# Performance work log

Measured on AMD Instinct MI355X. Metric: run time of the kernel, lower is better.

## Reference

```python
import jax, jax.numpy as jnp
import numpy as np

N, E, FS = 50000, 400000, 256
H, D = 8, 64            # GAT heads, hidden_size (per-head out_feats)
NH, DK, DV = 8, 64, 64  # transformer MHA
B = 1024
NEG_SLOPE = 0.2
EPS = 1e-6


def _layer_norm(x, g, b, eps=EPS):
    mu = x.mean(-1, keepdims=True)
    var = x.var(-1, keepdims=True)
    return (x - mu) / jnp.sqrt(var + eps) * g + b


def setup_inputs() -> dict:
    key = jax.random.key(0)
    ks = jax.random.split(key, 20)
    s = 0.02
    return {
        "features": jax.random.normal(ks[0], (N, FS), jnp.float32),
        "src": jax.random.randint(ks[1], (E,), 0, N, jnp.int32),
        "dst": jax.random.randint(ks[2], (E,), 0, N, jnp.int32),
        "url": jax.random.randint(ks[3], (B,), 1, N + 1, jnp.int32),  # 1-based ids
        # GATConv params (DGL-style)
        "gat_fc_w": jax.random.normal(ks[4], (FS, H * D), jnp.float32) * s,
        "attn_l": jax.random.normal(ks[5], (H, D), jnp.float32) * s,
        "attn_r": jax.random.normal(ks[6], (H, D), jnp.float32) * s,
        "gat_res_w": jax.random.normal(ks[7], (FS, H * D), jnp.float32) * s,
        "gat_bias": jnp.zeros((H, D), jnp.float32),
        # post-GAT LayerNorm
        "ln_g": jnp.ones((D,), jnp.float32),
        "ln_b": jnp.zeros((D,), jnp.float32),
        # MultiHeadAttention params
        "wq": jax.random.normal(ks[8], (D, NH * DK), jnp.float32) * s,
        "wk": jax.random.normal(ks[9], (D, NH * DK), jnp.float32) * s,
        "wv": jax.random.normal(ks[10], (D, NH * DV), jnp.float32) * s,
        "fc_w": jax.random.normal(ks[11], (NH * DV, D), jnp.float32) * s,
        "fc_b": jnp.zeros((D,), jnp.float32),
        "mha_ln_g": jnp.ones((D,), jnp.float32),
        "mha_ln_b": jnp.zeros((D,), jnp.float32),
        # final classifier
        "out_w": jax.random.normal(ks[12], (D, 2), jnp.float32) * s,
        "out_b": jnp.zeros((2,), jnp.float32),
    }


def reference(features, src, dst, url, gat_fc_w, attn_l, attn_r, gat_res_w,
              gat_bias, ln_g, ln_b, wq, wk, wv, fc_w, fc_b, mha_ln_g,
              mha_ln_b, out_w, out_b):
    # ---- GATConv (residual=True, bias, negative_slope=0.2, no activation) ----
    feat = (features @ gat_fc_w).reshape(N, H, D)          # [N,H,D]
    el = jnp.einsum('nhd,hd->nh', feat, attn_l)            # [N,H]
    er = jnp.einsum('nhd,hd->nh', feat, attn_r)            # [N,H]
    e = jax.nn.leaky_relu(el[src] + er[dst], NEG_SLOPE)    # [E,H] edge scores
    # segment softmax over incoming edges of each dst node
    m = jax.ops.segment_max(e, dst, num_segments=N)        # [N,H]
    m = jnp.where(jnp.isfinite(m), m, 0.0)
    ex = jnp.exp(e - m[dst])                               # [E,H]
    denom = jax.ops.segment_sum(ex, dst, num_segments=N)   # [N,H]
    a = ex / jnp.maximum(denom[dst], 1e-20)                # [E,H]
    msg = feat[src] * a[:, :, None]                        # [E,H,D]
    rst = jax.ops.segment_sum(msg, dst, num_segments=N)    # [N,H,D]
    res = (features @ gat_res_w).reshape(N, H, D)
    gat_emb = rst + res + gat_bias                         # [N,H,D]

    # ---- select batch nodes (url is 1-based) ----
    ids = url - 1
    x = gat_emb[ids]                                       # [B,H,D]
    x = _layer_norm(x, ln_g, ln_b)

    # ---- dense multi-head self-attention over the H gat heads (seq dim) ----
    residual = x
    q = (x @ wq).reshape(B, H, NH, DK)
    k = (x @ wk).reshape(B, H, NH, DK)
    v = (x @ wv).reshape(B, H, NH, DV)
    attn = jnp.einsum('bqhd,bkhd->bhqk', q, k) / jnp.sqrt(jnp.float32(DK))
    attn = jax.nn.softmax(attn, axis=-1)
    o = jnp.einsum('bhqk,bkhd->bqhd', attn, v).reshape(B, H, NH * DV)
    o = o @ fc_w + fc_b                                    # [B,H,D]
    o = _layer_norm(o + residual, mha_ln_g, mha_ln_b)

    # ---- pool + classify ----
    pooled = o.sum(axis=1)                                 # [B,D]
    logits = pooled @ out_w + out_b                        # [B,2]
    return logits
```

## Files before the change

kernel.cpp:

```cpp
#include <hip/hip_runtime.h>
#include <math.h>

#define Nn 50000
#define Ee 400000
#define FSz 256
#define HD_ 512
#define Bb 1024

static __device__ __forceinline__ int clampi(int v, int lo, int hi){
    return v < lo ? lo : (v > hi ? hi : v);
}
static __device__ __forceinline__ unsigned short f2bf(float f){
    unsigned int u = __float_as_uint(f);
    unsigned int r = u + 0x7FFFu + ((u >> 16) & 1u);
    return (unsigned short)(r >> 16);
}
static __device__ __forceinline__ float bflo(unsigned int v){ return __uint_as_float(v << 16); }
static __device__ __forceinline__ float bfhi(unsigned int v){ return __uint_as_float(v & 0xFFFF0000u); }

__global__ __launch_bounds__(256) void k_init(int* uid, int* fill, int* cnt,
                                              const float* __restrict__ W,
                                              const float* __restrict__ al,
                                              const float* __restrict__ ar,
                                              float* __restrict__ wl, float* __restrict__ wr){
    int t = threadIdx.x;
    if(blockIdx.x == 196){
        __shared__ float sal[512], sar[512];
        sal[t] = al[t]; sal[t+256] = al[t+256];
        sar[t] = ar[t]; sar[t+256] = ar[t+256];
        __syncthreads();
        const float4* Wr = (const float4*)(W + t*512);
        float accl[8] = {0,0,0,0,0,0,0,0};
        float accr[8] = {0,0,0,0,0,0,0,0};
        for(int i = 0; i < 128; i++){
            float4 w = Wr[i];
            int o = 4*i;
            int h = o >> 6;
            const float* alp = &sal[o];
            const float* arp = &sar[o];
            accl[h] += w.x*alp[0] + w.y*alp[1] + w.z*alp[2] + w.w*alp[3];
            accr[h] += w.x*arp[0] + w.y*arp[1] + w.z*arp[2] + w.w*arp[3];
        }
        #pragma unroll
        for(int h = 0; h < 8; h++){ wl[h*256 + t] = accl[h]; wr[h*256 + t] = accr[h]; }
    } else {
        int i = blockIdx.x * 256 + t;
        if(i < Nn) uid[i] = -1;
        if(i < 1024) fill[i] = 0;
        if(i == 0) cnt[0] = 0;
    }
}

__global__ __launch_bounds__(256) void k_mark(const int* __restrict__ url, int* uid, int* unode, int* cnt){
    int b = blockIdx.x * 256 + threadIdx.x;
    if(b >= Bb) return;
    int n = clampi(url[b] - 1, 0, Nn - 1);
    int old = atomicCAS(&uid[n], -1, -2);
    if(old == -1){
        int id = atomicAdd(cnt, 1);
        unode[id] = n;
        uid[n] = id;
    }
}

__global__ __launch_bounds__(256) void k_scatter(const int* __restrict__ src, const int* __restrict__ dst,
                                                 const int* __restrict__ uid, int* __restrict__ fill,
                                                 int* __restrict__ slist){
    int e = blockIdx.x * 256 + threadIdx.x;
    if(e >= Ee) return;
    int d = dst[e];
    if((unsigned)d >= (unsigned)Nn) return;
    int u = uid[d];
    if(u < 0) return;
    int pos = atomicAdd(&fill[u], 1);
    if(pos >= 64) return;
    slist[u*64 + pos] = clampi(src[e], 0, Nn - 1);
}

__global__ __launch_bounds__(256) void k_gat(const float* __restrict__ features,
                                             const float* __restrict__ Wfc,
                                             const float* __restrict__ Wres,
                                             const float* __restrict__ bias,
                                             const float* __restrict__ wl,
                                             const float* __restrict__ wr,
                                             const int* __restrict__ cnt, const int* __restrict__ unode,
                                             const int* __restrict__ fill, const int* __restrict__ slist,
                                             float* __restrict__ gemb){
    int t = threadIdx.x;
    int lane = t & 63, wv = t >> 6;
    int cntv = cnt[0];
    int u0 = blockIdx.x * 2;
    if(u0 >= cntv) return;

    __shared__ float swl[2048], swr[2048];
    __shared__ float cxs[2][8][256];
    __shared__ float fres[2][256];
    __shared__ float sew[2][64][8];
    __shared__ float ser[2][8];
    __shared__ int   sslist[2][64];

    for(int i = t; i < 2048; i += 256){ swl[i] = wl[i]; swr[i] = wr[i]; }

    int dg[2];
    dg[0] = min(fill[u0], 64);
    dg[1] = (u0 + 1 < cntv) ? min(fill[u0 + 1], 64) : 0;
    #pragma unroll
    for(int j = 0; j < 2; j++){
        int u = u0 + j;
        if(t < dg[j]) sslist[j][t] = slist[u*64 + t];
        if(u < cntv) fres[j][t] = features[(size_t)unode[u] * FSz + t];
        else         fres[j][t] = 0.f;
    }
    __syncthreads();

    int total = dg[0] + dg[1];
    for(int tau = wv; tau < total + 2; tau += 4){
        int j, i, s, isEr;
        if(tau < dg[0]){ j = 0; i = tau; s = sslist[0][i]; isEr = 0; }
        else if(tau < total){ j = 1; i = tau - dg[0]; s = sslist[1][i]; isEr = 0; }
        else { j = tau - total; i = 0; s = (u0 + j < cntv) ? unode[u0 + j] : 0; isEr = 1; }
        float4 x = *(const float4*)(features + (size_t)s * FSz + 4*lane);
        const float* Wt = isEr ? swr : swl;
        float p[8];
        #pragma unroll
        for(int h = 0; h < 8; h++){
            float4 w = *(const float4*)&Wt[h*256 + 4*lane];
            p[h] = x.x*w.x + x.y*w.y + x.z*w.z + x.w*w.w;
        }
        #pragma unroll
        for(int h = 0; h < 8; h++){
            #pragma unroll
            for(int m = 32; m >= 1; m >>= 1) p[h] += __shfl_xor(p[h], m, 64);
        }
        if(lane == 0){
            if(isEr){
                #pragma unroll
                for(int h = 0; h < 8; h++) ser[j][h] = p[h];
            } else {
                #pragma unroll
                for(int h = 0; h < 8; h++) sew[j][i][h] = p[h];
            }
        }
    }
    __syncthreads();
    if(t < 16){
        int j = t >> 3, h = t & 7;
        int dgj = dg[j];
        if(dgj > 0){
            float ern = ser[j][h];
            float m = -1e30f;
            for(int i = 0; i < dgj; i++){
                float v = sew[j][i][h] + ern;
                v = v > 0.f ? v : 0.2f * v;
                m = fmaxf(m, v);
            }
            float sum = 0.f;
            for(int i = 0; i < dgj; i++){
                float v = sew[j][i][h] + ern;
                v = v > 0.f ? v : 0.2f * v;
                float w = expf(v - m);
                sum += w;
                sew[j][i][h] = w;
            }
            float inv = 1.0f / fmaxf(sum, 1e-20f);
            for(int i = 0; i < dgj; i++) sew[j][i][h] *= inv;
        }
    }
    __syncthreads();
    #pragma unroll
    for(int j = 0; j < 2; j++){
        float cx[8] = {0,0,0,0,0,0,0,0};
        for(int i = 0; i < dg[j]; i++){
            int s = sslist[j][i];
            float x = features[(size_t)s * FSz + t];
            const float* av = &sew[j][i][0];
            #pragma unroll
            for(int h = 0; h < 8; h++) cx[h] += av[h] * x;
        }
        #pragma unroll
        for(int h = 0; h < 8; h++) cxs[j][h][t] = cx[h];
    }
    __syncthreads();

    int h = t >> 5;
    int o0 = 2 * t;
    const float2* Wfc2  = (const float2*)Wfc;
    const float2* Wres2 = (const float2*)Wres;
    float a00 = 0.f, a01 = 0.f, a10 = 0.f, a11 = 0.f;
    for(int f = 0; f < 256; f += 4){
        float2 w0 = Wfc2[(f+0)*256 + t];
        float2 w1 = Wfc2[(f+1)*256 + t];
        float2 w2 = Wfc2[(f+2)*256 + t];
        float2 w3 = Wfc2[(f+3)*256 + t];
        float2 r0 = Wres2[(f+0)*256 + t];
        float2 r1 = Wres2[(f+1)*256 + t];
        float2 r2 = Wres2[(f+2)*256 + t];
        float2 r3 = Wres2[(f+3)*256 + t];
        float4 c0 = *(const float4*)&cxs[0][h][f];
        float4 x0 = *(const float4*)&fres[0][f];
        float4 c1 = *(const float4*)&cxs[1][h][f];
        float4 x1 = *(const float4*)&fres[1][f];
        a00 += c0.x*w0.x + c0.y*w1.x + c0.z*w2.x + c0.w*w3.x + x0.x*r0.x + x0.y*r1.x + x0.z*r2.x + x0.w*r3.x;
        a01 += c0.x*w0.y + c0.y*w1.y + c0.z*w2.y + c0.w*w3.y + x0.x*r0.y + x0.y*r1.y + x0.z*r2.y + x0.w*r3.y;
        a10 += c1.x*w0.x + c1.y*w1.x + c1.z*w2.x + c1.w*w3.x + x1.x*r0.x + x1.y*r1.x + x1.z*r2.x + x1.w*r3.x;
        a11 += c1.x*w0.y + c1.y*w1.y + c1.z*w2.y + c1.w*w3.y + x1.x*r0.y + x1.y*r1.y + x1.z*r2.y + x1.w*r3.y;
    }
    float b0 = bias[o0], b1 = bias[o0 + 1];
    {
        float2* gp = (float2*)(gemb + (size_t)u0 * HD_);
        gp[t] = make_float2(a00 + b0, a01 + b1);
    }
    if(u0 + 1 < cntv){
        float2* gp = (float2*)(gemb + (size_t)(u0 + 1) * HD_);
        gp[t] = make_float2(a10 + b0, a11 + b1);
    }
}

__global__ __launch_bounds__(256, 6) void k_mha(const int* __restrict__ url, const int* __restrict__ uid,
                                             const float* __restrict__ gemb,
                                             const float* __restrict__ lng, const float* __restrict__ lnb,
                                             const float* __restrict__ wq, const float* __restrict__ wk,
                                             const float* __restrict__ wvp, const float* __restrict__ fcw,
                                             const float* __restrict__ fcb, const float* __restrict__ mlg,
                                             const float* __restrict__ mlb, const float* __restrict__ outw,
                                             const float* __restrict__ outb, float* __restrict__ out){
    __shared__ float A[512];
    __shared__ float xnF[512];
    __shared__ unsigned short xnT[64*8];
    __shared__ unsigned short qkb[2*8*520];
    __shared__ float mu8[8], rs8[8], pooled[64];

    int b = blockIdx.x, t = threadIdx.x;
    int lane = t & 63, wv = t >> 6;
    int n = clampi(url[b] - 1, 0, Nn - 1);
    int u = uid[n];
    if(u < 0) u = 0;
    const float* gp = gemb + (size_t)u * HD_;
    A[t] = gp[t]; A[t + 256] = gp[t + 256];
    __syncthreads();
    if(t < 8){
        float s = 0.f, s2 = 0.f;
        for(int d = 0; d < 64; d++){ float v = A[t*64 + d]; s += v; s2 += v * v; }
        float mu = s * (1.0f/64.0f);
        float var = s2 * (1.0f/64.0f) - mu * mu;
        mu8[t] = mu; rs8[t] = rsqrtf(fmaxf(var, 0.0f) + 1e-6f);
    }
    __syncthreads();
    #pragma unroll
    for(int p = 0; p < 2; p++){
        int i = p*256 + t; int q = i >> 6, d = i & 63;
        float xv = (A[i] - mu8[q]) * rs8[q] * lng[d] + lnb[d];
        xnF[i] = xv;
        xnT[d*8 + q] = f2bf(xv);
    }
    __syncthreads();
    float aq0[8] = {0,0,0,0,0,0,0,0}, aq1[8] = {0,0,0,0,0,0,0,0};
    float ak0[8] = {0,0,0,0,0,0,0,0}, ak1[8] = {0,0,0,0,0,0,0,0};
    #pragma unroll 4
    for(int d = 0; d < 64; d++){
        float q0 = wq[d*512 + t], q1 = wq[d*512 + t + 256];
        float k0 = wk[d*512 + t], k1 = wk[d*512 + t + 256];
        uint4 xp = *(const uint4*)&xnT[d*8];
        float xv[8] = { bflo(xp.x), bfhi(xp.x), bflo(xp.y), bfhi(xp.y),
                        bflo(xp.z), bfhi(xp.z), bflo(xp.w), bfhi(xp.w) };
        #pragma unroll
        for(int r = 0; r < 8; r++){
            aq0[r] += xv[r]*q0; aq1[r] += xv[r]*q1;
            ak0[r] += xv[r]*k0; ak1[r] += xv[r]*k1;
        }
    }
    #pragma unroll
    for(int qq = 0; qq < 8; qq++){
        qkb[qq*520 + t]              = f2bf(aq0[qq]);
        qkb[qq*520 + t + 256]        = f2bf(aq1[qq]);
        qkb[4160 + qq*520 + t]       = f2bf(ak0[qq]);
        qkb[4160 + qq*520 + t + 256] = f2bf(ak1[qq]);
    }
    __syncthreads();
    #pragma unroll
    for(int p = 0; p < 2; p++){
        int idx = p*256 + t;
        int nh = idx >> 6, qq = (idx >> 3) & 7, kk = idx & 7;
        const unsigned short* qrow = &qkb[qq*520 + nh*64];
        const unsigned short* krow = &qkb[4160 + kk*520 + nh*64];
        float s = 0.f;
        #pragma unroll
        for(int d8 = 0; d8 < 64; d8 += 8){
            uint4 qv = *(const uint4*)&qrow[d8];
            uint4 kv = *(const uint4*)&krow[d8];
            s += bflo(qv.x)*bflo(kv.x) + bfhi(qv.x)*bfhi(kv.x)
               + bflo(qv.y)*bflo(kv.y) + bfhi(qv.y)*bfhi(kv.y)
               + bflo(qv.z)*bflo(kv.z) + bfhi(qv.z)*bfhi(kv.z)
               + bflo(qv.w)*bflo(kv.w) + bfhi(qv.w)*bfhi(kv.w);
        }
        A[idx] = s * 0.125f;
    }
    __syncthreads();
    if(t < 64){
        float mx = -1e30f;
        #pragma unroll
        for(int k = 0; k < 8; k++) mx = fmaxf(mx, A[t*8 + k]);
        float e[8]; float s = 0.f;
        #pragma unroll
        for(int k = 0; k < 8; k++){ e[k] = expf(A[t*8 + k] - mx); s += e[k]; }
        float inv = 1.0f / s;
        #pragma unroll
        for(int k = 0; k < 8; k++) A[t*8 + k] = e[k] * inv;
    }
    __syncthreads();
    float av0[8] = {0,0,0,0,0,0,0,0}, av1[8] = {0,0,0,0,0,0,0,0};
    #pragma unroll 4
    for(int d = 0; d < 64; d++){
        float v0 = wvp[d*512 + t], v1 = wvp[d*512 + t + 256];
        uint4 xp = *(const uint4*)&xnT[d*8];
        float xv[8] = { bflo(xp.x), bfhi(xp.x), bflo(xp.y), bfhi(xp.y),
                        bflo(xp.z), bfhi(xp.z), bflo(xp.w), bfhi(xp.w) };
        #pragma unroll
        for(int r = 0; r < 8; r++){ av0[r] += xv[r]*v0; av1[r] += xv[r]*v1; }
    }
    {
        int nh0 = wv;
        #pragma unroll
        for(int qq = 0; qq < 8; qq++){
            const float* s0 = &A[nh0*64 + qq*8];
            const float* s1 = &A[(nh0+4)*64 + qq*8];
            float4 a0 = *(const float4*)s0, b0 = *(const float4*)(s0 + 4);
            float4 a1 = *(const float4*)s1, b1 = *(const float4*)(s1 + 4);
            float o0 = a0.x*av0[0] + a0.y*av0[1] + a0.z*av0[2] + a0.w*av0[3]
                     + b0.x*av0[4] + b0.y*av0[5] + b0.z*av0[6] + b0.w*av0[7];
            float o1 = a1.x*av1[0] + a1.y*av1[1] + a1.z*av1[2] + a1.w*av1[3]
                     + b1.x*av1[4] + b1.y*av1[5] + b1.z*av1[6] + b1.w*av1[7];
            qkb[qq*520 + t]       = f2bf(o0);
            qkb[qq*520 + t + 256] = f2bf(o1);
        }
    }
    __syncthreads();
    {
        float* P = (float*)&qkb[4160];
        int g = lane & 31;
        int qh = lane >> 5;
        int k0 = wv * 128;
        float a[4][2] = {{0,0},{0,0},{0,0},{0,0}};
        const float2* fw2 = (const float2*)fcw;
        for(int k = k0; k < k0 + 128; k += 8){
            float2 f0 = fw2[(k+0)*32 + g];
            float2 f1 = fw2[(k+1)*32 + g];
            float2 f2 = fw2[(k+2)*32 + g];
            float2 f3 = fw2[(k+3)*32 + g];
            float2 f4 = fw2[(k+4)*32 + g];
            float2 f5 = fw2[(k+5)*32 + g];
            float2 f6 = fw2[(k+6)*32 + g];
            float2 f7 = fw2[(k+7)*32 + g];
            #pragma unroll
            for(int jq = 0; jq < 4; jq++){
                int qq = qh*4 + jq;
                uint4 op = *(const uint4*)&qkb[qq*520 + k];
                float x0 = bflo(op.x), x1 = bfhi(op.x), x2 = bflo(op.y), x3 = bfhi(op.y);
                float x4 = bflo(op.z), x5 = bfhi(op.z), x6 = bflo(op.w), x7 = bfhi(op.w);
                a[jq][0] += x0*f0.x + x1*f1.x + x2*f2.x + x3*f3.x + x4*f4.x + x5*f5.x + x6*f6.x + x7*f7.x;
                a[jq][1] += x0*f0.y + x1*f1.y + x2*f2.y + x3*f3.y + x4*f4.y + x5*f5.y + x6*f6.y + x7*f7.y;
            }
        }
        __syncthreads();
        #pragma unroll
        for(int jq = 0; jq < 4; jq++){
            int qq = qh*4 + jq;
            *(float2*)&P[wv*512 + qq*64 + 2*g] = make_float2(a[jq][0], a[jq][1]);
        }
        __syncthreads();
        #pragma unroll
        for(int p = 0; p < 2; p++){
            int o = p*256 + t;
            int dd = o & 63;
            A[o] = P[o] + P[512 + o] + P[1024 + o] + P[1536 + o] + fcb[dd] + xnF[o];
        }
    }
    __syncthreads();
    if(t < 8){
        float s = 0.f, s2 = 0.f;
        for(int d = 0; d < 64; d++){ float v = A[t*64 + d]; s += v; s2 += v * v; }
        float mu = s * (1.0f/64.0f);
        float var = s2 * (1.0f/64.0f) - mu * mu;
        mu8[t] = mu; rs8[t] = rsqrtf(fmaxf(var, 0.0f) + 1e-6f);
    }
    __syncthreads();
    if(t < 64){
        float g2 = mlg[t], bb = mlb[t];
        float s = 0.f;
        #pragma unroll
        for(int qq = 0; qq < 8; qq++)
            s += (A[qq*64 + t] - mu8[qq]) * rs8[qq] * g2 + bb;
        pooled[t] = s;
    }
    __syncthreads();
    if(t < 2){
        float s = outb[t];
        for(int d = 0; d < 64; d++) s += pooled[d] * outw[d*2 + t];
        out[b*2 + t] = s;
    }
}

extern "C" void kernel_launch(void* const* d_in, const int* in_sizes, int n_in,
                              void* d_out, int out_size, void* d_ws, size_t ws_size,
                              hipStream_t stream){
    (void)in_sizes; (void)n_in; (void)out_size; (void)ws_size;
    const float* features  = (const float*)d_in[0];
    const int*   src       = (const int*)d_in[1];
    const int*   dst       = (const int*)d_in[2];
    const int*   url       = (const int*)d_in[3];
    const float* gat_fc_w  = (const float*)d_in[4];
    const float* attn_l    = (const float*)d_in[5];
    const float* attn_r    = (const float*)d_in[6];
    const float* gat_res_w = (const float*)d_in[7];
    const float* gat_bias  = (const float*)d_in[8];
    const float* ln_g      = (const float*)d_in[9];
    const float* ln_b      = (const float*)d_in[10];
    const float* wq        = (const float*)d_in[11];
    const float* wk        = (const float*)d_in[12];
    const float* wv        = (const float*)d_in[13];
    const float* fc_w      = (const float*)d_in[14];
    const float* fc_b      = (const float*)d_in[15];
    const float* mha_ln_g  = (const float*)d_in[16];
    const float* mha_ln_b  = (const float*)d_in[17];
    const float* out_w     = (const float*)d_in[18];
    const float* out_b     = (const float*)d_in[19];

    char* base = (char*)d_ws;
    size_t cur = 0;
    auto alloc = [&](size_t nbytes) -> void* {
        void* p = base + cur;
        cur = (cur + nbytes + 255) & ~(size_t)255;
        return p;
    };
    float* wl    = (float*)alloc(2048 * sizeof(float));
    float* wr    = (float*)alloc(2048 * sizeof(float));
    int*   uid   = (int*)alloc((size_t)Nn * sizeof(int));
    int*   unode = (int*)alloc(1024 * sizeof(int));
    int*   cnt   = (int*)alloc(16);
    int*   fill  = (int*)alloc(1024 * sizeof(int));
    int*   slist = (int*)alloc((size_t)1024 * 64 * sizeof(int));
    float* gemb  = (float*)alloc((size_t)1024 * 512 * sizeof(float));

    hipLaunchKernelGGL(k_init,    dim3(197),  dim3(256), 0, stream, uid, fill, cnt,
                       gat_fc_w, attn_l, attn_r, wl, wr);
    hipLaunchKernelGGL(k_mark,    dim3(4),    dim3(256), 0, stream, url, uid, unode, cnt);
    hipLaunchKernelGGL(k_scatter, dim3(1563), dim3(256), 0, stream, src, dst, uid, fill, slist);
    hipLaunchKernelGGL(k_gat,     dim3(512),  dim3(256), 0, stream, features, gat_fc_w, gat_res_w, gat_bias,
                       wl, wr, cnt, unode, fill, slist, gemb);
    hipLaunchKernelGGL(k_mha,     dim3(1024), dim3(256), 0, stream, url, uid, gemb, ln_g, ln_b,
                       wq, wk, wv, fc_w, fc_b, mha_ln_g, mha_ln_b, out_w, out_b,
                       (float*)d_out);
}
```

Baseline: 242.8 us.

## Merge init into mark, keep attention weights in registers, fuse V projection

Workspace initialisation moves from the k_init kernel to two hipMemsetAsync calls, and the attention-weight precompute moves into the k_mark launch, so one kernel launch is removed. In k_gat, the wl/wr vectors are held in per-lane registers instead of being staged through shared memory. In k_mha, the V projection is folded into the Q/K projection loop so x is read once, and launch bounds drop from 6 to 4 waves so the extra accumulators fit in registers. The trade-off is higher register pressure and lower occupancy in k_mha and k_gat, plus memset calls whose cost is not the same as a kernel's.

```diff
diff --git a/kernel.cpp b/kernel.cpp
--- a/kernel.cpp
+++ b/kernel.cpp
@@ -18,13 +18,13 @@
 static __device__ __forceinline__ float bflo(unsigned int v){ return __uint_as_float(v << 16); }
 static __device__ __forceinline__ float bfhi(unsigned int v){ return __uint_as_float(v & 0xFFFF0000u); }
 
-__global__ __launch_bounds__(256) void k_init(int* uid, int* fill, int* cnt,
+__global__ __launch_bounds__(256) void k_mark(const int* __restrict__ url, int* uid, int* unode, int* cnt,
                                               const float* __restrict__ W,
                                               const float* __restrict__ al,
                                               const float* __restrict__ ar,
                                               float* __restrict__ wl, float* __restrict__ wr){
     int t = threadIdx.x;
-    if(blockIdx.x == 196){
+    if(blockIdx.x == 4){
         __shared__ float sal[512], sar[512];
         sal[t] = al[t]; sal[t+256] = al[t+256];
         sar[t] = ar[t]; sar[t+256] = ar[t+256];
@@ -44,22 +44,16 @@
         #pragma unroll
         for(int h = 0; h < 8; h++){ wl[h*256 + t] = accl[h]; wr[h*256 + t] = accr[h]; }
     } else {
-        int i = blockIdx.x * 256 + t;
-        if(i < Nn) uid[i] = -1;
-        if(i < 1024) fill[i] = 0;
-        if(i == 0) cnt[0] = 0;
-    }
-}
-
-__global__ __launch_bounds__(256) void k_mark(const int* __restrict__ url, int* uid, int* unode, int* cnt){
-    int b = blockIdx.x * 256 + threadIdx.x;
-    if(b >= Bb) return;
-    int n = clampi(url[b] - 1, 0, Nn - 1);
-    int old = atomicCAS(&uid[n], -1, -2);
-    if(old == -1){
-        int id = atomicAdd(cnt, 1);
-        unode[id] = n;
-        uid[n] = id;
+        int b = blockIdx.x * 256 + t;
+        if(b < Bb){
+            int n = clampi(url[b] - 1, 0, Nn - 1);
+            int old = atomicCAS(&uid[n], -1, -2);
+            if(old == -1){
+                int id = atomicAdd(cnt, 1);
+                unode[id] = n;
+                uid[n] = id;
+            }
+        }
     }
 }
 
@@ -92,14 +86,18 @@
     int u0 = blockIdx.x * 2;
     if(u0 >= cntv) return;
 
-    __shared__ float swl[2048], swr[2048];
     __shared__ float cxs[2][8][256];
     __shared__ float fres[2][256];
     __shared__ float sew[2][64][8];
     __shared__ float ser[2][8];
     __shared__ int   sslist[2][64];
 
-    for(int i = t; i < 2048; i += 256){ swl[i] = wl[i]; swr[i] = wr[i]; }
+    float4 rwl[8], rwr[8];
+    #pragma unroll
+    for(int h = 0; h < 8; h++){
+        rwl[h] = *(const float4*)&wl[h*256 + 4*lane];
+        rwr[h] = *(const float4*)&wr[h*256 + 4*lane];
+    }
 
     int dg[2];
     dg[0] = min(fill[u0], 64);
@@ -120,12 +118,15 @@
         else if(tau < total){ j = 1; i = tau - dg[0]; s = sslist[1][i]; isEr = 0; }
         else { j = tau - total; i = 0; s = (u0 + j < cntv) ? unode[u0 + j] : 0; isEr = 1; }
         float4 x = *(const float4*)(features + (size_t)s * FSz + 4*lane);
-        const float* Wt = isEr ? swr : swl;
         float p[8];
-        #pragma unroll
-        for(int h = 0; h < 8; h++){
-            float4 w = *(const float4*)&Wt[h*256 + 4*lane];
-            p[h] = x.x*w.x + x.y*w.y + x.z*w.z + x.w*w.w;
+        if(isEr){
+            #pragma unroll
+            for(int h = 0; h < 8; h++)
+                p[h] = x.x*rwr[h].x + x.y*rwr[h].y + x.z*rwr[h].z + x.w*rwr[h].w;
+        } else {
+            #pragma unroll
+            for(int h = 0; h < 8; h++)
+                p[h] = x.x*rwl[h].x + x.y*rwl[h].y + x.z*rwl[h].z + x.w*rwl[h].w;
         }
         #pragma unroll
         for(int h = 0; h < 8; h++){
@@ -216,7 +217,7 @@
     }
 }
 
-__global__ __launch_bounds__(256, 6) void k_mha(const int* __restrict__ url, const int* __restrict__ uid,
+__global__ __launch_bounds__(256, 4) void k_mha(const int* __restrict__ url, const int* __restrict__ uid,
                                              const float* __restrict__ gemb,
                                              const float* __restrict__ lng, const float* __restrict__ lnb,
                                              const float* __restrict__ wq, const float* __restrict__ wk,
@@ -256,10 +257,12 @@
     __syncthreads();
     float aq0[8] = {0,0,0,0,0,0,0,0}, aq1[8] = {0,0,0,0,0,0,0,0};
     float ak0[8] = {0,0,0,0,0,0,0,0}, ak1[8] = {0,0,0,0,0,0,0,0};
-    #pragma unroll 4
+    float av0[8] = {0,0,0,0,0,0,0,0}, av1[8] = {0,0,0,0,0,0,0,0};
+    #pragma unroll 2
     for(int d = 0; d < 64; d++){
-        float q0 = wq[d*512 + t], q1 = wq[d*512 + t + 256];
-        float k0 = wk[d*512 + t], k1 = wk[d*512 + t + 256];
+        float q0 = wq[d*512 + t],  q1 = wq[d*512 + t + 256];
+        float k0 = wk[d*512 + t],  k1 = wk[d*512 + t + 256];
+        float v0 = wvp[d*512 + t], v1 = wvp[d*512 + t + 256];
         uint4 xp = *(const uint4*)&xnT[d*8];
         float xv[8] = { bflo(xp.x), bfhi(xp.x), bflo(xp.y), bfhi(xp.y),
                         bflo(xp.z), bfhi(xp.z), bflo(xp.w), bfhi(xp.w) };
@@ -267,6 +270,7 @@
         for(int r = 0; r < 8; r++){
             aq0[r] += xv[r]*q0; aq1[r] += xv[r]*q1;
             ak0[r] += xv[r]*k0; ak1[r] += xv[r]*k1;
+            av0[r] += xv[r]*v0; av1[r] += xv[r]*v1;
         }
     }
     #pragma unroll
@@ -308,16 +312,6 @@
         for(int k = 0; k < 8; k++) A[t*8 + k] = e[k] * inv;
     }
     __syncthreads();
-    float av0[8] = {0,0,0,0,0,0,0,0}, av1[8] = {0,0,0,0,0,0,0,0};
-    #pragma unroll 4
-    for(int d = 0; d < 64; d++){
-        float v0 = wvp[d*512 + t], v1 = wvp[d*512 + t + 256];
-        uint4 xp = *(const uint4*)&xnT[d*8];
-        float xv[8] = { bflo(xp.x), bfhi(xp.x), bflo(xp.y), bfhi(xp.y),
-                        bflo(xp.z), bfhi(xp.z), bflo(xp.w), bfhi(xp.w) };
-        #pragma unroll
-        for(int r = 0; r < 8; r++){ av0[r] += xv[r]*v0; av1[r] += xv[r]*v1; }
-    }
     {
         int nh0 = wv;
         #pragma unroll
@@ -436,14 +430,16 @@
     float* wr    = (float*)alloc(2048 * sizeof(float));
     int*   uid   = (int*)alloc((size_t)Nn * sizeof(int));
     int*   unode = (int*)alloc(1024 * sizeof(int));
-    int*   cnt   = (int*)alloc(16);
-    int*   fill  = (int*)alloc(1024 * sizeof(int));
+    int*   fill  = (int*)alloc(1056 * sizeof(int));
+    int*   cnt   = fill + 1024;
     int*   slist = (int*)alloc((size_t)1024 * 64 * sizeof(int));
     float* gemb  = (float*)alloc((size_t)1024 * 512 * sizeof(float));
 
-    hipLaunchKernelGGL(k_init,    dim3(197),  dim3(256), 0, stream, uid, fill, cnt,
+    hipMemsetAsync(uid, 0xFF, (size_t)Nn * sizeof(int), stream);
+    hipMemsetAsync(fill, 0, 1056 * sizeof(int), stream);
+
+    hipLaunchKernelGGL(k_mark,    dim3(5),    dim3(256), 0, stream, url, uid, unode, cnt,
                        gat_fc_w, attn_l, attn_r, wl, wr);
-    hipLaunchKernelGGL(k_mark,    dim3(4),    dim3(256), 0, stream, url, uid, unode, cnt);
     hipLaunchKernelGGL(k_scatter, dim3(1563), dim3(256), 0, stream, src, dst, uid, fill, slist);
     hipLaunchKernelGGL(k_gat,     dim3(512),  dim3(256), 0, stream, features, gat_fc_w, gat_res_w, gat_bias,
                        wl, wr, cnt, unode, fill, slist, gemb);
```

New measurement: 238.2 us. About the same (-1.9%).
